# Kernel tuning notes

Hardware: AMD Instinct MI355X
Metric: run time of the kernel (lower is better)

## Reference

```python
import jax, jax.numpy as jnp
import numpy as np

N_NODES = 50000
N_EDGES = 1600000
D = 128
LEAKY_SLOPE = 0.01  # torch nn.LeakyReLU default


def setup_inputs() -> dict:
    key = jax.random.key(0)
    ks = jax.random.split(key, 7)
    entity_embed = jax.random.normal(ks[0], (N_NODES, D), dtype=jnp.float32)
    W1 = jax.random.normal(ks[1], (D, D), dtype=jnp.float32) * 0.05
    b1 = jax.random.normal(ks[2], (D,), dtype=jnp.float32) * 0.05
    W2 = jax.random.normal(ks[3], (D, D), dtype=jnp.float32) * 0.05
    b2 = jax.random.normal(ks[4], (D,), dtype=jnp.float32) * 0.05
    src = jax.random.randint(ks[5], (N_EDGES,), 0, N_NODES, dtype=jnp.int32)
    dst = jax.random.randint(ks[6], (N_EDGES,), 0, N_NODES, dtype=jnp.int32)
    return {"entity_embed": entity_embed, "W1": W1, "b1": b1,
            "W2": W2, "b2": b2, "src": src, "dst": dst}


def reference(entity_embed, W1, b1, W2, b2, src, dst):
    # DGL update_all(copy_u('node','side'), sum('side','H')):
    # H[v] = sum over edges (u -> v) of entity_embed[u]
    n = entity_embed.shape[0]
    H = jax.ops.segment_sum(entity_embed[src], dst, num_segments=n)  # [N, D]
    # neighbors branch: LeakyReLU(W_1 @ H)
    neighbors = jax.nn.leaky_relu(H @ W1.T + b1, negative_slope=LEAKY_SLOPE)
    # interactions branch: LeakyReLU(W_2 @ (node * H))
    interactions = jax.nn.leaky_relu((entity_embed * H) @ W2.T + b2,
                                     negative_slope=LEAKY_SLOPE)
    # dropout is identity at inference
    return neighbors + interactions
```

## Files before the change

kernel.cpp:

```cpp
#include <hip/hip_runtime.h>

#define NN 50000
#define DD 128
#define SLOPE 0.01f
#define NB 782
#define BCAP 2560
#define ECH 6144
#define BST 512
#define PB 2
#define OVCAP 8192
#define HP 136

using bf16x8 = __attribute__((ext_vector_type(8))) short;
using f32x4  = __attribute__((ext_vector_type(4))) float;

__device__ inline float bflo(unsigned int w) { return __uint_as_float(w << 16); }
__device__ inline float bfhi(unsigned int w) { return __uint_as_float(w & 0xffff0000u); }
__device__ inline float sbf(short s) {
    return __uint_as_float(((unsigned int)(unsigned short)s) << 16);
}
__device__ inline unsigned int rnebf(float f) {
    unsigned int u = __float_as_uint(f);
    return (u + 0x7fffu + ((u >> 16) & 1u)) >> 16;
}
__device__ inline unsigned int pack2(float lo, float hi) {
    return rnebf(lo) | (rnebf(hi) << 16);
}
__device__ inline uint4 pack8f(const float* f) {
    uint4 o;
    o.x = pack2(f[0], f[1]); o.y = pack2(f[2], f[3]);
    o.z = pack2(f[4], f[5]); o.w = pack2(f[6], f[7]);
    return o;
}
__device__ inline void addrow(float* acc, uint4 r) {
    acc[0] += bflo(r.x); acc[1] += bfhi(r.x);
    acc[2] += bflo(r.y); acc[3] += bfhi(r.y);
    acc[4] += bflo(r.z); acc[5] += bfhi(r.z);
    acc[6] += bflo(r.w); acc[7] += bfhi(r.w);
}

__global__ __launch_bounds__(BST) void count_convert(
    const float* __restrict__ E, const float* __restrict__ W1,
    const float* __restrict__ W2, const int* __restrict__ dst,
    unsigned short* __restrict__ Ebf, unsigned short* __restrict__ W1b,
    unsigned short* __restrict__ W2b, int* __restrict__ cnt_g,
    int n_edges, int nbin)
{
    const int tid = threadIdx.x;

    if (blockIdx.x >= nbin) {
        const int NE8 = NN * DD / 8;
        const int NW8 = DD * DD / 8;
        int t = (blockIdx.x - nbin) * BST + tid;
        const float* s; unsigned short* d; int idx;
        if (t < NE8)                { s = E;  d = Ebf; idx = t; }
        else if (t < NE8 + NW8)     { s = W1; d = W1b; idx = t - NE8; }
        else if (t < NE8 + 2 * NW8) { s = W2; d = W2b; idx = t - NE8 - NW8; }
        else return;
        float4 a = ((const float4*)s)[(size_t)idx * 2];
        float4 b = ((const float4*)s)[(size_t)idx * 2 + 1];
        uint4 o;
        o.x = pack2(a.x, a.y); o.y = pack2(a.z, a.w);
        o.z = pack2(b.x, b.y); o.w = pack2(b.z, b.w);
        ((uint4*)d)[idx] = o;
        return;
    }

    __shared__ int cnt[NB];
    const int e0 = blockIdx.x * ECH;
    const int m = min(ECH, n_edges - e0);

    for (int b = tid; b < NB; b += BST) cnt[b] = 0;
    __syncthreads();
    for (int i = tid; i < m; i += BST)
        atomicAdd(&cnt[dst[e0 + i] >> 6], 1);
    __syncthreads();
    for (int b = tid; b < NB; b += BST)
        cnt_g[(size_t)b * nbin + blockIdx.x] = cnt[b];
}

__global__ __launch_bounds__(256) void scan_counts(
    int* __restrict__ cnt_g, int* __restrict__ gtail,
    int* __restrict__ ovf_cnt, int nbin)
{
    if (blockIdx.x == 0 && threadIdx.x == 0) *ovf_cnt = 0;
    const int w = threadIdx.x >> 6, lane = threadIdx.x & 63;
    const int bb = blockIdx.x * 4 + w;
    if (bb >= NB) return;
    int* row = cnt_g + (size_t)bb * nbin;
    int carry = 0;
    for (int base = 0; base < nbin; base += 64) {
        int blk = base + lane;
        int v = (blk < nbin) ? row[blk] : 0;
        int incl = v;
        #pragma unroll
        for (int d = 1; d < 64; d <<= 1) {
            int t = __shfl_up(incl, d);
            if (lane >= d) incl += t;
        }
        if (blk < nbin) row[blk] = carry + incl - v;
        carry += __shfl(incl, 63);
    }
    if (lane == 0) gtail[bb] = carry;
}

__global__ __launch_bounds__(BST) void scatter_edges(
    const int* __restrict__ src, const int* __restrict__ dst,
    const int* __restrict__ cnt_g, unsigned int* __restrict__ stag,
    int* __restrict__ ovf_cnt, int2* __restrict__ ovf,
    int n_edges, int nbin)
{
    __shared__ unsigned int srt[ECH];
    __shared__ int cnt[NB], off[NB], pos[NB], gbase[NB];
    __shared__ int wsum[BST / 64];

    const int tid = threadIdx.x;
    const int e0 = blockIdx.x * ECH;
    const int m = min(ECH, n_edges - e0);

    for (int b = tid; b < NB; b += BST) cnt[b] = 0;
    __syncthreads();

    for (int i = tid; i < m; i += BST)
        atomicAdd(&cnt[dst[e0 + i] >> 6], 1);
    for (int b = tid; b < NB; b += BST)
        gbase[b] = cnt_g[(size_t)b * nbin + blockIdx.x];
    __syncthreads();

    const int lane = tid & 63, w = tid >> 6;
    int b0 = tid * PB;
    int loc[PB]; int s = 0;
    #pragma unroll
    for (int j = 0; j < PB; ++j) {
        int bb = b0 + j;
        int cv = (bb < NB) ? cnt[bb] : 0;
        loc[j] = s; s += cv;
    }
    int incl = s;
    #pragma unroll
    for (int d = 1; d < 64; d <<= 1) {
        int t2 = __shfl_up(incl, d);
        if (lane >= d) incl += t2;
    }
    if (lane == 63) wsum[w] = incl;
    __syncthreads();
    int wbase = 0;
    for (int w2 = 0; w2 < w; ++w2) wbase += wsum[w2];
    int base = wbase + incl - s;
    #pragma unroll
    for (int j = 0; j < PB; ++j) {
        int bb = b0 + j;
        if (bb < NB) { off[bb] = base + loc[j]; pos[bb] = base + loc[j]; }
    }
    __syncthreads();

    for (int i = tid; i < m; i += BST) {
        int v = dst[e0 + i];
        int u = src[e0 + i];
        int bb = v >> 6;
        int p = atomicAdd(&pos[bb], 1);
        srt[p] = (unsigned int)u | ((unsigned int)(v & 63) << 16)
               | ((unsigned int)bb << 22);
    }
    __syncthreads();

    for (int i = tid; i < m; i += BST) {
        unsigned int r = srt[i];
        int bb = (int)(r >> 22);
        int gp = gbase[bb] + (i - off[bb]);
        if (gp < BCAP) {
            stag[(size_t)bb * BCAP + gp] = r & 0x3fffffu;
        } else {
            int oi = atomicAdd(ovf_cnt, 1);
            if (oi < OVCAP)
                ovf[oi] = make_int2((int)(r & 0xffffu),
                                    bb * 64 + (int)((r >> 16) & 63));
        }
    }
}

__global__ __launch_bounds__(256, 4) void bucket_fused(
    const unsigned short* __restrict__ Ebf, const int* __restrict__ gtail,
    const unsigned int* __restrict__ stag, const int* __restrict__ ovf_cnt,
    const int2* __restrict__ ovf,
    const unsigned short* __restrict__ W1b, const unsigned short* __restrict__ W2b,
    const float* __restrict__ b1, const float* __restrict__ b2,
    float* __restrict__ out)
{
    __shared__ unsigned short sorted[BCAP];
    __shared__ unsigned short Hs[64][HP];
    __shared__ int cnt[64], off[65], pos[64];
    __shared__ int s_novf;

    const int b = blockIdx.x;
    const int tid = threadIdx.x;
    int len = gtail[b]; len = len < BCAP ? len : BCAP;
    const unsigned int* seg = stag + (size_t)b * BCAP;

    if (tid == 0) { int t = *ovf_cnt; s_novf = t < OVCAP ? t : OVCAP; }
    if (tid < 64) cnt[tid] = 0;
    __syncthreads();
    for (int i = tid; i < len; i += 256)
        atomicAdd(&cnt[(seg[i] >> 16) & 63], 1);
    __syncthreads();
    if (tid < 64) {
        int cv = cnt[tid];
        int incl = cv;
        #pragma unroll
        for (int d = 1; d < 64; d <<= 1) {
            int t2 = __shfl_up(incl, d);
            if (tid >= d) incl += t2;
        }
        off[tid] = incl - cv;
        pos[tid] = incl - cv;
        if (tid == 63) off[64] = incl;
    }
    __syncthreads();
    for (int i = tid; i < len; i += 256) {
        unsigned int r = seg[i];
        int p = atomicAdd(&pos[(r >> 16) & 63], 1);
        sorted[p] = (unsigned short)(r & 0xffffu);
    }
    __syncthreads();
    const int novf = s_novf;

    const int g = tid >> 4;
    const int c = tid & 15;
    const uint4* E4 = (const uint4*)Ebf;
    for (int p4 = 0; p4 < 4; ++p4) {
        int nl = p4 * 16 + g;
        int v = b * 64 + nl;
        if (v >= NN) continue;
        float acc[8] = {};
        int i = off[nl], e1 = off[nl + 1];
        uint4 r[16];
        for (; i + 16 <= e1; i += 16) {
            #pragma unroll
            for (int k = 0; k < 16; ++k)
                r[k] = E4[(size_t)sorted[i + k] * 16 + c];
            __builtin_amdgcn_sched_barrier(0);
            #pragma unroll
            for (int k = 0; k < 16; ++k) addrow(acc, r[k]);
        }
        for (; i + 4 <= e1; i += 4) {
            #pragma unroll
            for (int k = 0; k < 4; ++k)
                r[k] = E4[(size_t)sorted[i + k] * 16 + c];
            __builtin_amdgcn_sched_barrier(0);
            #pragma unroll
            for (int k = 0; k < 4; ++k) addrow(acc, r[k]);
        }
        for (; i < e1; ++i) addrow(acc, E4[(size_t)sorted[i] * 16 + c]);

        if (novf > 0) {
            for (int k = 0; k < novf; ++k) {
                int2 e = ovf[k];
                if (e.y == v) addrow(acc, E4[(size_t)e.x * 16 + c]);
            }
        }
        *(uint4*)&Hs[nl][c * 8] = pack8f(acc);
    }
    __syncthreads();

    const int wave = tid >> 6;
    const int lane = tid & 63;
    const int v0 = b * 64 + wave * 16;
    if (v0 >= NN) return;
    const int m = lane & 15;
    const int quad = lane >> 4;

    bf16x8 aH[4], aE[4];
    const unsigned short* hrow = &Hs[wave * 16 + m][quad * 8];
    const unsigned short* erow = Ebf + (size_t)(v0 + m) * DD + quad * 8;
    #pragma unroll
    for (int ks = 0; ks < 4; ++ks) {
        bf16x8 h8 = *(const bf16x8*)(hrow + ks * 32);
        bf16x8 e8 = *(const bf16x8*)(erow + ks * 32);
        aH[ks] = h8;
        bf16x8 eh;
        #pragma unroll
        for (int j = 0; j < 8; ++j)
            eh[j] = (short)rnebf(sbf(h8[j]) * sbf(e8[j]));
        aE[ks] = eh;
    }

    #pragma unroll
    for (int jt = 0; jt < 8; ++jt) {
        const int j0 = jt * 16;
        const unsigned short* w1r = W1b + (size_t)(j0 + m) * DD + quad * 8;
        const unsigned short* w2r = W2b + (size_t)(j0 + m) * DD + quad * 8;
        f32x4 acc1 = {0.f, 0.f, 0.f, 0.f}, acc2 = {0.f, 0.f, 0.f, 0.f};
        #pragma unroll
        for (int ks = 0; ks < 4; ++ks) {
            bf16x8 bw1 = *(const bf16x8*)(w1r + ks * 32);
            bf16x8 bw2 = *(const bf16x8*)(w2r + ks * 32);
            acc1 = __builtin_amdgcn_mfma_f32_16x16x32_bf16(aH[ks], bw1, acc1, 0, 0, 0);
            acc2 = __builtin_amdgcn_mfma_f32_16x16x32_bf16(aE[ks], bw2, acc2, 0, 0, 0);
        }
        const float bb1 = b1[j0 + m], bb2 = b2[j0 + m];
        #pragma unroll
        for (int i = 0; i < 4; ++i) {
            int row = v0 + quad * 4 + i;
            if (row < NN) {
                float x1 = acc1[i] + bb1; x1 = x1 > 0.f ? x1 : SLOPE * x1;
                float x2 = acc2[i] + bb2; x2 = x2 > 0.f ? x2 : SLOPE * x2;
                out[(size_t)row * DD + j0 + m] = x1 + x2;
            }
        }
    }
}

__global__ __launch_bounds__(256) void scatter_add(
    const float* __restrict__ E, const int* __restrict__ src,
    const int* __restrict__ dst, float* __restrict__ H, int n_edges)
{
    int t = blockIdx.x * 256 + threadIdx.x;
    int e = t >> 5;
    if (e >= n_edges) return;
    int c = t & 31;
    float4 a = ((const float4*)E)[(size_t)src[e] * 32 + c];
    float* hp = H + (size_t)dst[e] * DD + c * 4;
    atomicAdd(hp + 0, a.x); atomicAdd(hp + 1, a.y);
    atomicAdd(hp + 2, a.z); atomicAdd(hp + 3, a.w);
}

__global__ __launch_bounds__(256) void fused_mlp(
    const float* __restrict__ E, const float* __restrict__ H,
    const float* __restrict__ W1, const float* __restrict__ b1,
    const float* __restrict__ W2, const float* __restrict__ b2,
    float* __restrict__ out)
{
    __shared__ float Hsf[32][DD];
    __shared__ float EHs[32][DD];
    __shared__ float W1s[DD][20];
    __shared__ float W2s[DD][20];
    const int tid = threadIdx.x;
    const int v0 = blockIdx.x * 32;
    const int nvalid = min(32, NN - v0);
    for (int i = 0; i < 4; ++i) {
        int f = tid + 256 * i;
        int n = f >> 5, c = f & 31;
        float4 h = make_float4(0.f, 0.f, 0.f, 0.f);
        float4 eh = h;
        if (n < nvalid) {
            h = ((const float4*)H)[(size_t)(v0 + n) * 32 + c];
            float4 e4 = ((const float4*)E)[(size_t)(v0 + n) * 32 + c];
            eh = make_float4(e4.x * h.x, e4.y * h.y, e4.z * h.z, e4.w * h.w);
        }
        *((float4*)&Hsf[n][c * 4]) = h;
        *((float4*)&EHs[n][c * 4]) = eh;
    }
    const int jg = tid & 63;
    const int n0 = (tid >> 6) * 8;
    float acc1a[8] = {}, acc1b[8] = {}, acc2a[8] = {}, acc2b[8] = {};
    for (int t8 = 0; t8 < 8; ++t8) {
        const int k0 = t8 * 16;
        __syncthreads();
        for (int i = 0; i < 8; ++i) {
            int f = tid + 256 * i;
            int j = f >> 4, kk = f & 15;
            W1s[j][kk] = W1[j * DD + k0 + kk];
            W2s[j][kk] = W2[j * DD + k0 + kk];
        }
        __syncthreads();
        for (int c = 0; c < 4; ++c) {
            float4 w1a = *((const float4*)&W1s[jg][c * 4]);
            float4 w1b = *((const float4*)&W1s[jg + 64][c * 4]);
            float4 w2a = *((const float4*)&W2s[jg][c * 4]);
            float4 w2b = *((const float4*)&W2s[jg + 64][c * 4]);
            const int kk = k0 + c * 4;
            for (int n = 0; n < 8; ++n) {
                float4 h = *((const float4*)&Hsf[n0 + n][kk]);
                float4 eh = *((const float4*)&EHs[n0 + n][kk]);
                acc1a[n] += h.x * w1a.x + h.y * w1a.y + h.z * w1a.z + h.w * w1a.w;
                acc1b[n] += h.x * w1b.x + h.y * w1b.y + h.z * w1b.z + h.w * w1b.w;
                acc2a[n] += eh.x * w2a.x + eh.y * w2a.y + eh.z * w2a.z + eh.w * w2a.w;
                acc2b[n] += eh.x * w2b.x + eh.y * w2b.y + eh.z * w2b.z + eh.w * w2b.w;
            }
        }
    }
    const float b1a = b1[jg], b1b = b1[jg + 64];
    const float b2a = b2[jg], b2b = b2[jg + 64];
    for (int n = 0; n < 8; ++n) {
        if (n0 + n < nvalid) {
            const int v = v0 + n0 + n;
            float x1 = acc1a[n] + b1a; x1 = x1 > 0.f ? x1 : SLOPE * x1;
            float x2 = acc2a[n] + b2a; x2 = x2 > 0.f ? x2 : SLOPE * x2;
            out[(size_t)v * DD + jg] = x1 + x2;
            float y1 = acc1b[n] + b1b; y1 = y1 > 0.f ? y1 : SLOPE * y1;
            float y2 = acc2b[n] + b2b; y2 = y2 > 0.f ? y2 : SLOPE * y2;
            out[(size_t)v * DD + jg + 64] = y1 + y2;
        }
    }
}

extern "C" void kernel_launch(void* const* d_in, const int* in_sizes, int n_in,
                              void* d_out, int out_size, void* d_ws, size_t ws_size,
                              hipStream_t stream)
{
    const float* E  = (const float*)d_in[0];
    const float* W1 = (const float*)d_in[1];
    const float* b1 = (const float*)d_in[2];
    const float* W2 = (const float*)d_in[3];
    const float* b2 = (const float*)d_in[4];
    const int* src  = (const int*)d_in[5];
    const int* dst  = (const int*)d_in[6];
    float* out = (float*)d_out;
    const int n_edges = in_sizes[5];

    char* ws = (char*)d_ws;
    auto al = [](size_t x) { return (x + 255) & ~(size_t)255; };

    const int nbin = (n_edges + ECH - 1) / ECH;

    const size_t off_tail = 0;
    const size_t off_ovfc = (size_t)NB * 4;
    const size_t off_ovf  = al(off_ovfc + 4);
    const size_t off_stag = al(off_ovf + (size_t)OVCAP * 8);
    const size_t off_Ebf  = al(off_stag + (size_t)NB * BCAP * 4);
    const size_t off_W1b  = al(off_Ebf + (size_t)NN * DD * 2);
    const size_t off_W2b  = al(off_W1b + (size_t)DD * DD * 2);
    const size_t off_cntg = al(off_W2b + (size_t)DD * DD * 2);
    const size_t need_bf  = off_cntg + (size_t)NB * nbin * 4;

    if (ws_size >= need_bf) {
        int*  gtail   = (int*)(ws + off_tail);
        int*  ovf_cnt = (int*)(ws + off_ovfc);
        int2* ovf     = (int2*)(ws + off_ovf);
        unsigned int*   stag = (unsigned int*)(ws + off_stag);
        unsigned short* Ebf  = (unsigned short*)(ws + off_Ebf);
        unsigned short* W1b  = (unsigned short*)(ws + off_W1b);
        unsigned short* W2b  = (unsigned short*)(ws + off_W2b);
        int*  cnt_g   = (int*)(ws + off_cntg);

        const int ncv  = NN * DD / 8 + 2 * (DD * DD / 8);
        const int ncvb = (ncv + BST - 1) / BST;

        count_convert<<<nbin + ncvb, BST, 0, stream>>>(
            E, W1, W2, dst, Ebf, W1b, W2b, cnt_g, n_edges, nbin);
        scan_counts<<<(NB + 3) / 4, 256, 0, stream>>>(
            cnt_g, gtail, ovf_cnt, nbin);
        scatter_edges<<<nbin, BST, 0, stream>>>(
            src, dst, cnt_g, stag, ovf_cnt, ovf, n_edges, nbin);
        bucket_fused<<<NB, 256, 0, stream>>>(
            Ebf, gtail, stag, ovf_cnt, ovf, W1b, W2b, b1, b2, out);
        return;
    }

    const size_t hbytes = (size_t)NN * DD * sizeof(float);
    float* H = (ws_size >= hbytes) ? (float*)ws : out;
    hipMemsetAsync(H, 0, hbytes, stream);
    scatter_add<<<((n_edges * 32) + 255) / 256, 256, 0, stream>>>(
        E, src, dst, H, n_edges);
    fused_mlp<<<(NN + 31) / 32, 256, 0, stream>>>(E, H, W1, b1, W2, b2, out);
}
```

Baseline: 196.8 us.

## Gather neighbor rows one node per wave with 4-byte lanes instead of 16-lane groups

The gather-sum phase now has each wave handle its own 16 destination nodes sequentially. Each lane loads one 32-bit word (two bf16) of a source row, where before a 16-thread group loaded 16-byte chunks across four node passes. Because each wave then reads only the H rows it wrote itself, the block-wide barrier before the MFMA stage is dropped. The trade-off is more, smaller load instructions per row and possible load imbalance between waves, in exchange for fewer live registers, no cross-wave sync and per-wave locality.

Result: no change. 196.8 us (+0.0%).

```diff
diff --git a/kernel.cpp b/kernel.cpp
--- a/kernel.cpp
+++ b/kernel.cpp
@@ -25,18 +25,6 @@
 }
 __device__ inline unsigned int pack2(float lo, float hi) {
     return rnebf(lo) | (rnebf(hi) << 16);
-}
-__device__ inline uint4 pack8f(const float* f) {
-    uint4 o;
-    o.x = pack2(f[0], f[1]); o.y = pack2(f[2], f[3]);
-    o.z = pack2(f[4], f[5]); o.w = pack2(f[6], f[7]);
-    return o;
-}
-__device__ inline void addrow(float* acc, uint4 r) {
-    acc[0] += bflo(r.x); acc[1] += bfhi(r.x);
-    acc[2] += bflo(r.y); acc[3] += bfhi(r.y);
-    acc[4] += bflo(r.z); acc[5] += bfhi(r.z);
-    acc[6] += bflo(r.w); acc[7] += bfhi(r.w);
 }
 
 __global__ __launch_bounds__(BST) void count_convert(
@@ -194,6 +182,8 @@
 
     const int b = blockIdx.x;
     const int tid = threadIdx.x;
+    const int wave = tid >> 6;
+    const int lane = tid & 63;
     int len = gtail[b]; len = len < BCAP ? len : BCAP;
     const unsigned int* seg = stag + (size_t)b * BCAP;
 
@@ -224,46 +214,46 @@
     __syncthreads();
     const int novf = s_novf;
 
-    const int g = tid >> 4;
-    const int c = tid & 15;
-    const uint4* E4 = (const uint4*)Ebf;
-    for (int p4 = 0; p4 < 4; ++p4) {
-        int nl = p4 * 16 + g;
-        int v = b * 64 + nl;
-        if (v >= NN) continue;
-        float acc[8] = {};
+    const unsigned int* E1 = (const unsigned int*)Ebf;
+    for (int s16 = 0; s16 < 16; ++s16) {
+        const int nl = wave * 16 + s16;
+        const int v = b * 64 + nl;
+        if (v >= NN) break;
+        float a0 = 0.f, a1 = 0.f;
         int i = off[nl], e1 = off[nl + 1];
-        uint4 r[16];
+        unsigned int r[16];
         for (; i + 16 <= e1; i += 16) {
             #pragma unroll
             for (int k = 0; k < 16; ++k)
-                r[k] = E4[(size_t)sorted[i + k] * 16 + c];
+                r[k] = E1[(size_t)sorted[i + k] * 64 + lane];
             __builtin_amdgcn_sched_barrier(0);
             #pragma unroll
-            for (int k = 0; k < 16; ++k) addrow(acc, r[k]);
+            for (int k = 0; k < 16; ++k) { a0 += bflo(r[k]); a1 += bfhi(r[k]); }
         }
         for (; i + 4 <= e1; i += 4) {
             #pragma unroll
             for (int k = 0; k < 4; ++k)
-                r[k] = E4[(size_t)sorted[i + k] * 16 + c];
+                r[k] = E1[(size_t)sorted[i + k] * 64 + lane];
             __builtin_amdgcn_sched_barrier(0);
             #pragma unroll
-            for (int k = 0; k < 4; ++k) addrow(acc, r[k]);
-        }
-        for (; i < e1; ++i) addrow(acc, E4[(size_t)sorted[i] * 16 + c]);
-
+            for (int k = 0; k < 4; ++k) { a0 += bflo(r[k]); a1 += bfhi(r[k]); }
+        }
+        for (; i < e1; ++i) {
+            unsigned int r0 = E1[(size_t)sorted[i] * 64 + lane];
+            a0 += bflo(r0); a1 += bfhi(r0);
+        }
         if (novf > 0) {
             for (int k = 0; k < novf; ++k) {
                 int2 e = ovf[k];
-                if (e.y == v) addrow(acc, E4[(size_t)e.x * 16 + c]);
+                if (e.y == v) {
+                    unsigned int r0 = E1[(size_t)e.x * 64 + lane];
+                    a0 += bflo(r0); a1 += bfhi(r0);
+                }
             }
         }
-        *(uint4*)&Hs[nl][c * 8] = pack8f(acc);
-    }
-    __syncthreads();
-
-    const int wave = tid >> 6;
-    const int lane = tid & 63;
+        *(unsigned int*)&Hs[nl][lane * 2] = pack2(a0, a1);
+    }
+
     const int v0 = b * 64 + wave * 16;
     if (v0 >= NN) return;
     const int m = lane & 15;
```
